# Kernel optimization log

Measured on AMD Instinct MI355X. Metric: run time of the kernel, lower is better.

Reference implementation:

```python
import jax, jax.numpy as jnp
import numpy as np

N = 100_000      # num nodes
E = 100_000      # num hyperedges
NNZ = 1_600_000  # incidence entries (avg degree 16)
DIN = 128
DOUT = 128


def setup_inputs() -> dict:
    key = jax.random.key(0)
    k1, k2, k3, k4 = jax.random.split(key, 4)
    x = jax.random.normal(k1, (N, DIN), dtype=jnp.float32)
    weight = jax.random.normal(k2, (DIN, DOUT), dtype=jnp.float32) / np.sqrt(DIN).astype(np.float32)
    bias = jax.random.normal(k3, (DOUT,), dtype=jnp.float32) * 0.02
    hyperedge_index = jax.random.randint(k4, (2, NNZ), 0, N, dtype=jnp.int64)
    return {"x": x, "weight": weight, "bias": bias, "hyperedge_index": hyperedge_index}


def reference(x, weight, bias, hyperedge_index):
    # PyG HypergraphConv (use_attention=False, heads=1):
    #   out = D^{-1} H W B^{-1} H^T (x @ Theta) + bias, W = I (unit hyperedge weights)
    node_idx = hyperedge_index[0]  # [NNZ]
    edge_idx = hyperedge_index[1]  # [NNZ]

    h = x @ weight  # [N, DOUT]

    ones = jnp.ones((NNZ,), dtype=h.dtype)
    # node degree D_i = sum of hyperedge weights (=1) over incident hyperedges
    D = jax.ops.segment_sum(ones, node_idx, num_segments=N)   # [N]
    # hyperedge degree B_e = number of incident nodes
    B = jax.ops.segment_sum(ones, edge_idx, num_segments=E)   # [E]
    Dinv = jnp.where(D > 0, 1.0 / D, 0.0)
    Binv = jnp.where(B > 0, 1.0 / B, 0.0)

    # nodes -> hyperedges: m_e = B_e^{-1} * sum_{i in e} h_i
    e_feat = jax.ops.segment_sum(h[node_idx], edge_idx, num_segments=E) * Binv[:, None]  # [E, DOUT]
    # hyperedges -> nodes: out_i = D_i^{-1} * sum_{e ni i} m_e
    out = jax.ops.segment_sum(e_feat[edge_idx], node_idx, num_segments=N) * Dinv[:, None]  # [N, DOUT]
    return out + bias
```

## Files before the change

### kernel.cpp

```cpp
#include <hip/hip_runtime.h>

#define Nn 100000
#define Ne 100000
#define NNZC 1600000
#define NBLK 256
#define CHUNK 6250
#define BSH 8
#define NBK 391
#define CAPB 5120
#define GEMM_TOTAL 391
#define LCAP 2816
#define NHB 782

typedef __attribute__((ext_vector_type(8))) short short8;
typedef __attribute__((ext_vector_type(4))) float floatx4;

__device__ inline unsigned short f2bf(float f) {
    union { float f; unsigned int i; } c; c.f = f;
    unsigned int i = c.i;
    return (unsigned short)((i + 0x7fffu + ((i >> 16) & 1u)) >> 16);
}
__device__ inline unsigned int f2bf2(float lo, float hi) {
    union { float f; unsigned int i; } a, b;
    a.f = lo; b.f = hi;
    const unsigned int x = (a.i + 0x7fffu + ((a.i >> 16) & 1u)) >> 16;
    const unsigned int y = (b.i + 0x7fffu + ((b.i >> 16) & 1u)) & 0xffff0000u;
    return x | y;
}

union FusedLds {
    unsigned short wlds[128 * 136];
    struct { int a[NBK]; int b[NBK]; } s;
};

__device__ inline void gemm_block256(int gb, const float* __restrict__ x,
                                     const float* __restrict__ w,
                                     unsigned short* __restrict__ h,
                                     unsigned short* wlds, int tid) {
    const int wave = tid >> 6, lane = tid & 63;
    const int q = lane >> 4, r16 = lane & 15;

    for (int i = tid; i < 4096; i += 256) {
        const int k = i >> 5;
        const int n0 = (i & 31) << 2;
        const float4 wv = *(const float4*)(w + k * 128 + n0);
        wlds[(n0 + 0) * 136 + k] = f2bf(wv.x);
        wlds[(n0 + 1) * 136 + k] = f2bf(wv.y);
        wlds[(n0 + 2) * 136 + k] = f2bf(wv.z);
        wlds[(n0 + 3) * 136 + k] = f2bf(wv.w);
    }
    __syncthreads();

#pragma unroll 1
    for (int rg = 0; rg < 4; ++rg) {
        const int row0 = gb * 256 + rg * 64 + wave * 16;
        const int rrow = min(row0 + r16, Nn - 1);

        floatx4 acc[8];
#pragma unroll
        for (int jb = 0; jb < 8; ++jb) acc[jb] = (floatx4){0.f, 0.f, 0.f, 0.f};

        const float* ap = x + (size_t)rrow * 128 + q * 8;
#pragma unroll
        for (int kk = 0; kk < 4; ++kk) {
            const float4 a0 = *(const float4*)(ap + kk * 32);
            const float4 a1 = *(const float4*)(ap + kk * 32 + 4);
            union { unsigned int u[4]; short8 s; } xf;
            xf.u[0] = f2bf2(a0.x, a0.y);
            xf.u[1] = f2bf2(a0.z, a0.w);
            xf.u[2] = f2bf2(a1.x, a1.y);
            xf.u[3] = f2bf2(a1.z, a1.w);
            const unsigned short* wp = wlds + kk * 32 + q * 8;
#pragma unroll
            for (int jb = 0; jb < 8; ++jb) {
                const short8 wf = *(const short8*)(wp + (jb * 16 + r16) * 136);
                acc[jb] = __builtin_amdgcn_mfma_f32_16x16x32_bf16(wf, xf.s, acc[jb], 0, 0, 0);
            }
        }

        if (row0 + r16 < Nn) {
            unsigned short* hb = h + (size_t)(row0 + r16) * 128 + q * 4;
#pragma unroll
            for (int jb = 0; jb < 8; ++jb) {
                uint2 o;
                o.x = f2bf2(acc[jb][0], acc[jb][1]);
                o.y = f2bf2(acc[jb][2], acc[jb][3]);
                *(uint2*)(hb + jb * 16) = o;
            }
        }
    }
}

__global__ __launch_bounds__(256) void scatter_gemm_kernel(
        const int* __restrict__ nidx, const int* __restrict__ eidx,
        int* __restrict__ gcurN, int* __restrict__ gcurE,
        unsigned int* __restrict__ pairsN, unsigned int* __restrict__ pairsE,
        const float* __restrict__ x, const float* __restrict__ w,
        unsigned short* __restrict__ h) {
    __shared__ FusedLds sm;
    const int tid = threadIdx.x;
    if (blockIdx.x < NBLK) {
        for (int j = tid; j < NBK; j += 256) { sm.s.a[j] = 0; sm.s.b[j] = 0; }
        __syncthreads();
        const int base = blockIdx.x * CHUNK;
        for (int i = base + tid; i < base + CHUNK; i += 256) {
            atomicAdd(&sm.s.a[nidx[i] >> BSH], 1);
            atomicAdd(&sm.s.b[eidx[i] >> BSH], 1);
        }
        __syncthreads();
        for (int j = tid; j < NBK; j += 256) {
            sm.s.a[j] = atomicAdd(&gcurN[j], sm.s.a[j]);
            sm.s.b[j] = atomicAdd(&gcurE[j], sm.s.b[j]);
        }
        __syncthreads();
        for (int i = base + tid; i < base + CHUNK; i += 256) {
            const int n = nidx[i], e = eidx[i];
            const int pn = atomicAdd(&sm.s.a[n >> BSH], 1);
            if (pn < CAPB)
                pairsN[(size_t)(n >> BSH) * CAPB + pn] =
                    ((unsigned int)e << 8) | (unsigned int)(n & 255);
            const int pe = atomicAdd(&sm.s.b[e >> BSH], 1);
            if (pe < CAPB)
                pairsE[(size_t)(e >> BSH) * CAPB + pe] =
                    ((unsigned int)n << 8) | (unsigned int)(e & 255);
        }
    } else {
        gemm_block256(blockIdx.x - NBLK, x, w, h, sm.wlds, tid);
    }
}

template <int MODE>
__global__ __launch_bounds__(512) void bucketgather_kernel(
        const unsigned int* __restrict__ pairs, const int* __restrict__ gcur,
        const void* __restrict__ srcv, const float* __restrict__ bias,
        void* __restrict__ outv) {
    __shared__ int perm_lds[LCAP];
    __shared__ int offs_lds[129];
    __shared__ int cnt[128];
    __shared__ int cur[128];
    __shared__ int tmp[2][128];
    const int b = blockIdx.x >> 1;
    const int half = blockIdx.x & 1;
    const int tid = threadIdx.x;
    const int wave = tid >> 6, lane = tid & 63;

    const int fill = min(gcur[b], CAPB);
    const unsigned int* pb = pairs + (size_t)b * CAPB;

    if (tid < 128) cnt[tid] = 0;
    __syncthreads();
    for (int i = tid; i < fill; i += 512) {
        const unsigned int p = pb[i];
        if ((int)((p >> 7) & 1u) == half) atomicAdd(&cnt[p & 127u], 1);
    }
    __syncthreads();
    int v = 0, pin = 0;
    if (tid < 128) { v = cnt[tid]; tmp[0][tid] = v; }
    for (int off = 1; off < 128; off <<= 1) {
        __syncthreads();
        if (tid < 128) {
            int val = tmp[pin][tid];
            if (tid >= off) val += tmp[pin][tid - off];
            tmp[1 - pin][tid] = val;
        }
        pin ^= 1;
    }
    __syncthreads();
    if (tid < 128) {
        const int excl = tmp[pin][tid] - v;
        offs_lds[tid] = excl;
        cur[tid] = excl;
        if (tid == 127) offs_lds[128] = tmp[pin][127];
    }
    __syncthreads();
    for (int i = tid; i < fill; i += 512) {
        const unsigned int p = pb[i];
        if ((int)((p >> 7) & 1u) == half) {
            const int pos = atomicAdd(&cur[p & 127u], 1);
            if (pos < LCAP) perm_lds[pos] = (int)(p >> 8);
        }
    }
    __syncthreads();

    const int i0 = wave << 4;
    const int start = offs_lds[i0];
    const int end = offs_lds[i0 + 16];
    const int pmax = min(offs_lds[128], LCAP) - 1;
    const unsigned int l4 = (unsigned int)lane << 2;
    const char* src = (const char*)srcv;

    float bx = 0.f, by = 0.f;
    if (MODE == 1) {
        const float2 bb = ((const float2*)bias)[lane];
        bx = bb.x; by = bb.y;
    }

    float ax = 0.f, ay = 0.f;
    int e = i0;
    int seg_start = start;
    int nb = offs_lds[i0 + 1];
    const int gidbase = (b << 8) + (half << 7);

    auto flush = [&](int deg) {
        const int gid = gidbase + e;
        if (gid < 100000) {
            const float sinv = deg ? 1.f / (float)deg : 0.f;
            if (MODE == 0) {
                *(unsigned int*)((char*)outv + (((size_t)gid) << 8) + l4) =
                    f2bf2(ax * sinv, ay * sinv);
            } else {
                float2 o;
                o.x = ax * sinv + bx;
                o.y = ay * sinv + by;
                *(float2*)((char*)outv + (((size_t)gid) << 9) + ((size_t)l4 << 1)) = o;
            }
        }
        ax = 0.f; ay = 0.f;
        ++e;
    };

    int myv = 0;
    for (int i = start; i < end; i += 8) {
        const int t = (i - start) & 63;
        if (t == 0) myv = perm_lds[min(i + lane, pmax)];
        const int m = min(end - i, 8);
        unsigned int a[8], u[8];
#pragma unroll
        for (int j = 0; j < 8; ++j)
            a[j] = ((unsigned int)__shfl(myv, t + (j < m ? j : m - 1), 64) << 8) | l4;
#pragma unroll
        for (int j = 0; j < 8; ++j) u[j] = *(const unsigned int*)(src + a[j]);
#pragma unroll
        for (int j = 0; j < 8; ++j) {
            if (j < m) {
                while (i + j == nb) {
                    flush(nb - seg_start);
                    seg_start = nb;
                    nb = offs_lds[e + 1];
                }
                ax += __uint_as_float(u[j] << 16);
                ay += __uint_as_float(u[j] & 0xffff0000u);
            }
        }
    }
    while (e < i0 + 16) {
        flush(end - seg_start);
        seg_start = end;
    }
}

extern "C" void kernel_launch(void* const* d_in, const int* in_sizes, int n_in,
                              void* d_out, int out_size, void* d_ws, size_t ws_size,
                              hipStream_t stream) {
    const float* x = (const float*)d_in[0];
    const float* w = (const float*)d_in[1];
    const float* bias = (const float*)d_in[2];
    const int* hei = (const int*)d_in[3];
    const int* nidx = hei;
    const int* eidx = hei + NNZC;
    float* out = (float*)d_out;

    char* p = (char*)d_ws;
    unsigned short* h = (unsigned short*)p;  p += (size_t)Nn * 128 * 2;
    unsigned short* ef = (unsigned short*)p; p += (size_t)Ne * 128 * 2;
    int* gcurN = (int*)p;                    p += NBK * 4 + 192;
    int* gcurE = (int*)p;                    p += NBK * 4 + 192;
    unsigned int* pairsN = (unsigned int*)p; p += (size_t)NBK * CAPB * 4;
    unsigned int* pairsE = (unsigned int*)p; p += (size_t)NBK * CAPB * 4;

    hipMemsetAsync(gcurN, 0, 2 * (NBK * 4 + 192), stream);

    scatter_gemm_kernel<<<NBLK + GEMM_TOTAL, 256, 0, stream>>>(nidx, eidx, gcurN, gcurE,
                                                               pairsN, pairsE, x, w, h);
    bucketgather_kernel<0><<<NHB, 512, 0, stream>>>(pairsE, gcurE, h, nullptr, ef);
    bucketgather_kernel<1><<<NHB, 512, 0, stream>>>(pairsN, gcurN, ef, bias, out);
}
```

Measured before the change: 308.6 us.

## Split fused scatter/GEMM kernel and gather buckets across quarter blocks

Separates the fused scatter and GEMM into two kernels and replaces the half-bucket 512-thread gather with quarter-bucket 256-thread blocks with a swizzled block index. The intent is finer-grained gather parallelism and smaller LDS per block for better occupancy and load balance. In exchange, each bucket's pair list is scanned four times instead of twice, and the scatter and GEMM no longer run concurrently within one launch.

```diff
diff --git a/kernel.cpp b/kernel.cpp
--- a/kernel.cpp
+++ b/kernel.cpp
@@ -9,8 +9,8 @@
 #define NBK 391
 #define CAPB 5120
 #define GEMM_TOTAL 391
-#define LCAP 2816
-#define NHB 782
+#define LCAP 1408
+#define NQB 1568
 
 typedef __attribute__((ext_vector_type(8))) short short8;
 typedef __attribute__((ext_vector_type(4))) float floatx4;
@@ -28,17 +28,46 @@
     return x | y;
 }
 
-union FusedLds {
-    unsigned short wlds[128 * 136];
-    struct { int a[NBK]; int b[NBK]; } s;
-};
-
-__device__ inline void gemm_block256(int gb, const float* __restrict__ x,
-                                     const float* __restrict__ w,
-                                     unsigned short* __restrict__ h,
-                                     unsigned short* wlds, int tid) {
+__global__ __launch_bounds__(256) void scatter_kernel(
+        const int* __restrict__ nidx, const int* __restrict__ eidx,
+        int* __restrict__ gcurN, int* __restrict__ gcurE,
+        unsigned int* __restrict__ pairsN, unsigned int* __restrict__ pairsE) {
+    __shared__ struct { int a[NBK]; int b[NBK]; } sm;
+    const int tid = threadIdx.x;
+    for (int j = tid; j < NBK; j += 256) { sm.a[j] = 0; sm.b[j] = 0; }
+    __syncthreads();
+    const int base = blockIdx.x * CHUNK;
+    for (int i = base + tid; i < base + CHUNK; i += 256) {
+        atomicAdd(&sm.a[nidx[i] >> BSH], 1);
+        atomicAdd(&sm.b[eidx[i] >> BSH], 1);
+    }
+    __syncthreads();
+    for (int j = tid; j < NBK; j += 256) {
+        sm.a[j] = atomicAdd(&gcurN[j], sm.a[j]);
+        sm.b[j] = atomicAdd(&gcurE[j], sm.b[j]);
+    }
+    __syncthreads();
+    for (int i = base + tid; i < base + CHUNK; i += 256) {
+        const int n = nidx[i], e = eidx[i];
+        const int pn = atomicAdd(&sm.a[n >> BSH], 1);
+        if (pn < CAPB)
+            pairsN[(size_t)(n >> BSH) * CAPB + pn] =
+                ((unsigned int)e << 8) | (unsigned int)(n & 255);
+        const int pe = atomicAdd(&sm.b[e >> BSH], 1);
+        if (pe < CAPB)
+            pairsE[(size_t)(e >> BSH) * CAPB + pe] =
+                ((unsigned int)n << 8) | (unsigned int)(e & 255);
+    }
+}
+
+__global__ __launch_bounds__(256) void gemm_kernel(
+        const float* __restrict__ x, const float* __restrict__ w,
+        unsigned short* __restrict__ h) {
+    __shared__ unsigned short wlds[128 * 136];
+    const int tid = threadIdx.x;
     const int wave = tid >> 6, lane = tid & 63;
     const int q = lane >> 4, r16 = lane & 15;
+    const int gb = blockIdx.x;
 
     for (int i = tid; i < 4096; i += 256) {
         const int k = i >> 5;
@@ -91,74 +120,39 @@
     }
 }
 
-__global__ __launch_bounds__(256) void scatter_gemm_kernel(
-        const int* __restrict__ nidx, const int* __restrict__ eidx,
-        int* __restrict__ gcurN, int* __restrict__ gcurE,
-        unsigned int* __restrict__ pairsN, unsigned int* __restrict__ pairsE,
-        const float* __restrict__ x, const float* __restrict__ w,
-        unsigned short* __restrict__ h) {
-    __shared__ FusedLds sm;
-    const int tid = threadIdx.x;
-    if (blockIdx.x < NBLK) {
-        for (int j = tid; j < NBK; j += 256) { sm.s.a[j] = 0; sm.s.b[j] = 0; }
-        __syncthreads();
-        const int base = blockIdx.x * CHUNK;
-        for (int i = base + tid; i < base + CHUNK; i += 256) {
-            atomicAdd(&sm.s.a[nidx[i] >> BSH], 1);
-            atomicAdd(&sm.s.b[eidx[i] >> BSH], 1);
-        }
-        __syncthreads();
-        for (int j = tid; j < NBK; j += 256) {
-            sm.s.a[j] = atomicAdd(&gcurN[j], sm.s.a[j]);
-            sm.s.b[j] = atomicAdd(&gcurE[j], sm.s.b[j]);
-        }
-        __syncthreads();
-        for (int i = base + tid; i < base + CHUNK; i += 256) {
-            const int n = nidx[i], e = eidx[i];
-            const int pn = atomicAdd(&sm.s.a[n >> BSH], 1);
-            if (pn < CAPB)
-                pairsN[(size_t)(n >> BSH) * CAPB + pn] =
-                    ((unsigned int)e << 8) | (unsigned int)(n & 255);
-            const int pe = atomicAdd(&sm.s.b[e >> BSH], 1);
-            if (pe < CAPB)
-                pairsE[(size_t)(e >> BSH) * CAPB + pe] =
-                    ((unsigned int)n << 8) | (unsigned int)(e & 255);
-        }
-    } else {
-        gemm_block256(blockIdx.x - NBLK, x, w, h, sm.wlds, tid);
-    }
-}
-
 template <int MODE>
-__global__ __launch_bounds__(512) void bucketgather_kernel(
+__global__ __launch_bounds__(256) void quartergather_kernel(
         const unsigned int* __restrict__ pairs, const int* __restrict__ gcur,
         const void* __restrict__ srcv, const float* __restrict__ bias,
         void* __restrict__ outv) {
     __shared__ int perm_lds[LCAP];
-    __shared__ int offs_lds[129];
-    __shared__ int cnt[128];
-    __shared__ int cur[128];
-    __shared__ int tmp[2][128];
-    const int b = blockIdx.x >> 1;
-    const int half = blockIdx.x & 1;
+    __shared__ int offs_lds[65];
+    __shared__ int cnt[64];
+    __shared__ int cur[64];
+    __shared__ int tmp[2][64];
+    const int v = blockIdx.x;
+    const int xs = v & 7, j = v >> 3;
+    const int qq = j & 3;
+    const int b = xs + ((j >> 2) << 3);
+    if (b >= NBK) return;
     const int tid = threadIdx.x;
     const int wave = tid >> 6, lane = tid & 63;
 
     const int fill = min(gcur[b], CAPB);
     const unsigned int* pb = pairs + (size_t)b * CAPB;
 
-    if (tid < 128) cnt[tid] = 0;
-    __syncthreads();
-    for (int i = tid; i < fill; i += 512) {
+    if (tid < 64) cnt[tid] = 0;
+    __syncthreads();
+    for (int i = tid; i < fill; i += 256) {
         const unsigned int p = pb[i];
-        if ((int)((p >> 7) & 1u) == half) atomicAdd(&cnt[p & 127u], 1);
-    }
-    __syncthreads();
-    int v = 0, pin = 0;
-    if (tid < 128) { v = cnt[tid]; tmp[0][tid] = v; }
-    for (int off = 1; off < 128; off <<= 1) {
+        if ((int)((p >> 6) & 3u) == qq) atomicAdd(&cnt[p & 63u], 1);
+    }
+    __syncthreads();
+    int vv = 0, pin = 0;
+    if (tid < 64) { vv = cnt[tid]; tmp[0][tid] = vv; }
+    for (int off = 1; off < 64; off <<= 1) {
         __syncthreads();
-        if (tid < 128) {
+        if (tid < 64) {
             int val = tmp[pin][tid];
             if (tid >= off) val += tmp[pin][tid - off];
             tmp[1 - pin][tid] = val;
@@ -166,17 +160,17 @@
         pin ^= 1;
     }
     __syncthreads();
-    if (tid < 128) {
-        const int excl = tmp[pin][tid] - v;
+    if (tid < 64) {
+        const int excl = tmp[pin][tid] - vv;
         offs_lds[tid] = excl;
         cur[tid] = excl;
-        if (tid == 127) offs_lds[128] = tmp[pin][127];
-    }
-    __syncthreads();
-    for (int i = tid; i < fill; i += 512) {
+        if (tid == 63) offs_lds[64] = tmp[pin][63];
+    }
+    __syncthreads();
+    for (int i = tid; i < fill; i += 256) {
         const unsigned int p = pb[i];
-        if ((int)((p >> 7) & 1u) == half) {
-            const int pos = atomicAdd(&cur[p & 127u], 1);
+        if ((int)((p >> 6) & 3u) == qq) {
+            const int pos = atomicAdd(&cur[p & 63u], 1);
             if (pos < LCAP) perm_lds[pos] = (int)(p >> 8);
         }
     }
@@ -184,8 +178,8 @@
 
     const int i0 = wave << 4;
     const int start = offs_lds[i0];
-    const int end = offs_lds[i0 + 16];
-    const int pmax = min(offs_lds[128], LCAP) - 1;
+    const int end = min(offs_lds[i0 + 16], LCAP);
+    const int pmax = min(offs_lds[64], LCAP) - 1;
     const unsigned int l4 = (unsigned int)lane << 2;
     const char* src = (const char*)srcv;
 
@@ -199,7 +193,7 @@
     int e = i0;
     int seg_start = start;
     int nb = offs_lds[i0 + 1];
-    const int gidbase = (b << 8) + (half << 7);
+    const int gidbase = (b << 8) + (qq << 6);
 
     auto flush = [&](int deg) {
         const int gid = gidbase + e;
@@ -226,20 +220,20 @@
         const int m = min(end - i, 8);
         unsigned int a[8], u[8];
 #pragma unroll
-        for (int j = 0; j < 8; ++j)
-            a[j] = ((unsigned int)__shfl(myv, t + (j < m ? j : m - 1), 64) << 8) | l4;
-#pragma unroll
-        for (int j = 0; j < 8; ++j) u[j] = *(const unsigned int*)(src + a[j]);
-#pragma unroll
-        for (int j = 0; j < 8; ++j) {
-            if (j < m) {
-                while (i + j == nb) {
+        for (int jj = 0; jj < 8; ++jj)
+            a[jj] = ((unsigned int)__shfl(myv, t + (jj < m ? jj : m - 1), 64) << 8) | l4;
+#pragma unroll
+        for (int jj = 0; jj < 8; ++jj) u[jj] = *(const unsigned int*)(src + a[jj]);
+#pragma unroll
+        for (int jj = 0; jj < 8; ++jj) {
+            if (jj < m) {
+                while (i + jj == nb) {
                     flush(nb - seg_start);
                     seg_start = nb;
                     nb = offs_lds[e + 1];
                 }
-                ax += __uint_as_float(u[j] << 16);
-                ay += __uint_as_float(u[j] & 0xffff0000u);
+                ax += __uint_as_float(u[jj] << 16);
+                ay += __uint_as_float(u[jj] & 0xffff0000u);
             }
         }
     }
@@ -270,8 +264,8 @@
 
     hipMemsetAsync(gcurN, 0, 2 * (NBK * 4 + 192), stream);
 
-    scatter_gemm_kernel<<<NBLK + GEMM_TOTAL, 256, 0, stream>>>(nidx, eidx, gcurN, gcurE,
-                                                               pairsN, pairsE, x, w, h);
-    bucketgather_kernel<0><<<NHB, 512, 0, stream>>>(pairsE, gcurE, h, nullptr, ef);
-    bucketgather_kernel<1><<<NHB, 512, 0, stream>>>(pairsN, gcurN, ef, bias, out);
-}
+    scatter_kernel<<<NBLK, 256, 0, stream>>>(nidx, eidx, gcurN, gcurE, pairsN, pairsE);
+    gemm_kernel<<<GEMM_TOTAL, 256, 0, stream>>>(x, w, h);
+    quartergather_kernel<0><<<NQB, 256, 0, stream>>>(pairsE, gcurE, h, nullptr, ef);
+    quartergather_kernel<1><<<NQB, 256, 0, stream>>>(pairsN, gcurN, ef, bias, out);
+}
```

Result: slower. 321.2 us (+4.1%).
